# Kernel tuning notes

Hardware: AMD Instinct MI355X
Metric: run time of the kernel (lower is better)

Reference implementation:

```python
import jax, jax.numpy as jnp
import numpy as np

N, E, H, HEADS, NC, BLK = 100000, 1600000, 128, 4, 8192, 128

def _layernorm(x, g, b, eps=1e-5):
    m = jnp.mean(x, axis=-1, keepdims=True)
    v = jnp.var(x, axis=-1, keepdims=True)
    return (x - m) * jax.lax.rsqrt(v + eps) * g + b

def setup_inputs() -> dict:
    key = jax.random.key(0)
    ks = jax.random.split(key, 24)
    s = 0.05
    p = lambda k, shp: jax.random.normal(k, shp, jnp.float32) * s
    return {
        'x': jax.random.normal(ks[0], (N, H), jnp.float32),
        'ea': jax.random.normal(ks[1], (E, H), jnp.float32),
        # GINEConv edge linear (edge_dim -> hidden)
        'We': p(ks[2], (H, H)), 'be_': p(ks[3], (H,)),
        # GINEConv mlp: Linear(H,H) -> ReLU -> Linear(H,H)
        'W1': p(ks[4], (H, H)), 'b1': p(ks[5], (H,)),
        'W2': p(ks[6], (H, H)), 'b2': p(ks[7], (H,)),
        'ln1_g': jnp.ones((H,), jnp.float32), 'ln1_b': jnp.zeros((H,), jnp.float32),
        # MultiheadAttention packed qkv + out proj
        'in_w': p(ks[8], (3 * H, H)), 'in_b': p(ks[9], (3 * H,)),
        'out_w': p(ks[10], (H, H)), 'out_b': p(ks[11], (H,)),
        'ln2_g': jnp.ones((H,), jnp.float32), 'ln2_b': jnp.zeros((H,), jnp.float32),
        # FFN: Linear(H,2H) -> ReLU -> Linear(2H,H)
        'f1_w': p(ks[12], (2 * H, H)), 'f1_b': p(ks[13], (2 * H,)),
        'f2_w': p(ks[14], (H, 2 * H)), 'f2_b': p(ks[15], (H,)),
        'ei': jax.random.randint(ks[16], (2, E), 0, N, jnp.int64),
        'chem_idx': jnp.arange(NC, dtype=jnp.int64),
        'B': BLK,
    }

def reference(x, ea, We, be_, W1, b1, W2, b2, ln1_g, ln1_b, in_w, in_b,
              out_w, out_b, ln2_g, ln2_b, f1_w, f1_b, f2_w, f2_b,
              ei, chem_idx, B):
    n = x.shape[0]
    # ---- GINEConv: out_i = mlp((1+eps)*x_i + sum_j relu(x_j + lin(e_ji))), eps=0 ----
    src, dst = ei[0], ei[1]
    msg = jax.nn.relu(x[src] + ea @ We.T + be_)          # [E, H]
    agg = jax.ops.segment_sum(msg, dst, num_segments=n)  # [N, H]
    h = agg + x
    h = jax.nn.relu(h @ W1.T + b1) @ W2.T + b2
    x = _layernorm(x + h, ln1_g, ln1_b)
    # ---- chunked self-attention over chem nodes (chunks of size B) ----
    xc = x[chem_idx].reshape(-1, B, x.shape[-1])         # [nc, B, H]
    nc, _, hid = xc.shape
    dh = hid // HEADS
    qkv = xc @ in_w.T + in_b                             # [nc, B, 3H]
    q, k, v = jnp.split(qkv, 3, axis=-1)
    sp = lambda t: t.reshape(nc, B, HEADS, dh)
    att = jax.nn.softmax(jnp.einsum('bqhd,bkhd->bhqk', sp(q), sp(k)) * (1.0 / np.sqrt(dh)).astype(np.float32), axis=-1)
    o = jnp.einsum('bhqk,bkhd->bqhd', att, sp(v)).reshape(nc, B, hid)
    xc = xc + (o @ out_w.T + out_b)                      # residual inside BlockMHA
    xc = xc.reshape(-1, hid)
    # ---- FFN on chem subset ----
    h2 = _layernorm(xc, ln2_g, ln2_b)
    xc = xc + (jax.nn.relu(h2 @ f1_w.T + f1_b) @ f2_w.T + f2_b)
    return x.at[chem_idx].set(xc)
```

## Files before the change

### kernel.cpp

```cpp
#include <hip/hip_runtime.h>
#include <hip/hip_bf16.h>
#include <math.h>

typedef __attribute__((ext_vector_type(8))) __bf16 bf16x8;
typedef __attribute__((ext_vector_type(4))) float f32x4;
typedef __attribute__((ext_vector_type(4))) unsigned short u16x4;

#define HD  128
#define LDP 136

__device__ __forceinline__ unsigned short f2bf(float f) {
  __bf16 h = (__bf16)f;
  union { __bf16 h; unsigned short u; } v; v.h = h; return v.u;
}
__device__ __forceinline__ float bf2f(unsigned short h) {
  union { unsigned u; float f; } v; v.u = ((unsigned)h) << 16; return v.f;
}

__device__ __forceinline__ int idx_at(const void* p, long long i, int is64) {
  if (is64) return (int)((const long long*)p)[i];
  return ((const int*)p)[i];
}

__device__ __forceinline__ void mfma_tile_128(const unsigned short* a_s,
                                              const unsigned short* w_s,
                                              int w, int l15, int lg,
                                              f32x4 acc[2][8]) {
#pragma unroll
  for (int kk = 0; kk < 4; ++kk) {
    bf16x8 a[2], b[8];
#pragma unroll
    for (int mt = 0; mt < 2; ++mt)
      a[mt] = *(const bf16x8*)&a_s[(w * 32 + mt * 16 + l15) * LDP + kk * 32 + lg * 8];
#pragma unroll
    for (int nt = 0; nt < 8; ++nt)
      b[nt] = *(const bf16x8*)&w_s[(nt * 16 + l15) * LDP + kk * 32 + lg * 8];
#pragma unroll
    for (int mt = 0; mt < 2; ++mt)
#pragma unroll
      for (int nt = 0; nt < 8; ++nt)
        acc[mt][nt] = __builtin_amdgcn_mfma_f32_16x16x32_bf16(a[mt], b[nt], acc[mt][nt], 0, 0, 0);
  }
}

__device__ __forceinline__ void stage_f32(unsigned short* dst, const float* src,
                                          long long src_ld, int tid) {
  for (int i = tid; i < 128 * 32; i += 256) {
    int r = i >> 5, c = (i & 31) << 2;
    float4 f = *(const float4*)&src[(long long)r * src_ld + c];
    u16x4 h = { f2bf(f.x), f2bf(f.y), f2bf(f.z), f2bf(f.w) };
    *(u16x4*)&dst[r * LDP + c] = h;
  }
}

__global__ void detect_idx_kernel(const void* __restrict__ ei, int E, int N,
                                  int* __restrict__ flag) {
  if (threadIdx.x == 0 && blockIdx.x == 0) {
    const long long* p = (const long long*)ei;
    int is64 = 1;
    long long step = E / 64; if (step < 1) step = 1;
    for (int i = 0; i < 64; ++i) {
      long long v = p[i * step];
      if (v < 0 || v >= N) { is64 = 0; break; }
    }
    *flag = is64;
  }
}

__global__ __launch_bounds__(256) void hist_kernel(const void* __restrict__ ei,
                                                   const int* __restrict__ flag,
                                                   int* __restrict__ deg, int E) {
  const int is64 = *flag;
  for (long long e = blockIdx.x * 256LL + threadIdx.x; e < E;
       e += (long long)gridDim.x * 256)
    atomicAdd(&deg[idx_at(ei, (long long)E + e, is64)], 1);
}

#define SCH 1024
__global__ __launch_bounds__(256) void scan_a(const int* __restrict__ deg,
                                              int* __restrict__ bsum, int N) {
  const int b = blockIdx.x, t = threadIdx.x;
  int p = 0;
#pragma unroll
  for (int k = 0; k < 4; ++k) {
    int idx = b * SCH + t * 4 + k;
    if (idx < N) p += deg[idx];
  }
  __shared__ int warr[4];
  for (int o = 32; o > 0; o >>= 1) p += __shfl_xor(p, o);
  if ((t & 63) == 0) warr[t >> 6] = p;
  __syncthreads();
  if (t == 0) bsum[b] = warr[0] + warr[1] + warr[2] + warr[3];
}
__global__ void scan_b(int* __restrict__ bsum, int* __restrict__ off, int NB, int N) {
  if (threadIdx.x == 0 && blockIdx.x == 0) {
    int run = 0;
    for (int b = 0; b < NB; ++b) { int t = bsum[b]; bsum[b] = run; run += t; }
    off[N] = run;
  }
}
__global__ __launch_bounds__(256) void scan_c(const int* __restrict__ deg,
                                              const int* __restrict__ bsum,
                                              int* __restrict__ off,
                                              int* __restrict__ cursor, int N) {
  const int b = blockIdx.x, t = threadIdx.x;
  int d[4], s = 0;
#pragma unroll
  for (int k = 0; k < 4; ++k) {
    int idx = b * SCH + t * 4 + k;
    d[k] = (idx < N) ? deg[idx] : 0;
    s += d[k];
  }
  __shared__ int arr[256];
  arr[t] = s;
  __syncthreads();
  for (int stp = 1; stp < 256; stp <<= 1) {
    int v = (t >= stp) ? arr[t - stp] : 0;
    __syncthreads();
    arr[t] += v;
    __syncthreads();
  }
  int base = bsum[b] + arr[t] - s;
  int acc = 0;
#pragma unroll
  for (int k = 0; k < 4; ++k) {
    int idx = b * SCH + t * 4 + k;
    if (idx < N) { off[idx] = base + acc; cursor[idx] = base + acc; }
    acc += d[k];
  }
}

__global__ __launch_bounds__(256, 3) void edge_kernel4(
    const float* __restrict__ x, const float* __restrict__ ea,
    const float* __restrict__ We, const float* __restrict__ be,
    const void* __restrict__ ei, const int* __restrict__ flag,
    int* __restrict__ cursor, unsigned short* __restrict__ msg, int E, int N) {
  __shared__ unsigned short we_s[128 * LDP];
  __shared__ int s_src[128];
  __shared__ int s_pos[128];
  const int tid = threadIdx.x;
  const long long e0 = (long long)blockIdx.x * 128;
  const int is64 = *flag;

  if (tid < 128) {
    long long e = e0 + tid;
    int s = 0, p = 0;
    if (e < E) {
      s = idx_at(ei, e, is64);
      int d = idx_at(ei, (long long)E + e, is64);
      p = atomicAdd(&cursor[d], 1);
    }
    s_src[tid] = s; s_pos[tid] = p;
  }

  const int lane = tid & 63, w = tid >> 6;
  const int l15 = lane & 15, lg = lane >> 4;

  float4 af[2][4][2];
#pragma unroll
  for (int mt = 0; mt < 2; ++mt) {
    long long row = e0 + w * 32 + mt * 16 + l15;
    const float* src = &ea[(row < E ? row : e0) * HD + lg * 8];
#pragma unroll
    for (int kk = 0; kk < 4; ++kk) {
      af[mt][kk][0] = *(const float4*)&src[kk * 32];
      af[mt][kk][1] = *(const float4*)&src[kk * 32 + 4];
    }
  }

  for (int i = tid; i < 128 * 32; i += 256) {
    int r = i >> 5, c = (i & 31) << 2;
    float4 g = *(const float4*)&We[r * HD + c];
    u16x4 hw = { f2bf(g.x), f2bf(g.y), f2bf(g.z), f2bf(g.w) };
    *(u16x4*)&we_s[r * LDP + c] = hw;
  }

  bf16x8 a[2][4];
#pragma unroll
  for (int mt = 0; mt < 2; ++mt)
#pragma unroll
    for (int kk = 0; kk < 4; ++kk) {
      float4 f0 = af[mt][kk][0], f1 = af[mt][kk][1];
      bf16x8 t;
      t[0] = (__bf16)f0.x; t[1] = (__bf16)f0.y; t[2] = (__bf16)f0.z; t[3] = (__bf16)f0.w;
      t[4] = (__bf16)f1.x; t[5] = (__bf16)f1.y; t[6] = (__bf16)f1.z; t[7] = (__bf16)f1.w;
      a[mt][kk] = t;
    }
  __syncthreads();

  f32x4 acc[2][8];
#pragma unroll
  for (int mt = 0; mt < 2; ++mt)
#pragma unroll
    for (int nt = 0; nt < 8; ++nt) acc[mt][nt] = (f32x4){0.f, 0.f, 0.f, 0.f};

#pragma unroll
  for (int kk = 0; kk < 4; ++kk) {
    bf16x8 b[8];
#pragma unroll
    for (int nt = 0; nt < 8; ++nt)
      b[nt] = *(const bf16x8*)&we_s[(nt * 16 + l15) * LDP + kk * 32 + lg * 8];
#pragma unroll
    for (int mt = 0; mt < 2; ++mt)
#pragma unroll
      for (int nt = 0; nt < 8; ++nt)
        acc[mt][nt] = __builtin_amdgcn_mfma_f32_16x16x32_bf16(a[mt][kk], b[nt], acc[mt][nt], 0, 0, 0);
  }

  float bev[8];
#pragma unroll
  for (int nt = 0; nt < 8; ++nt) bev[nt] = be[nt * 16 + l15];
  __syncthreads();

#pragma unroll
  for (int mt = 0; mt < 2; ++mt) {
#pragma unroll
    for (int r = 0; r < 4; ++r) {
      int m = w * 32 + mt * 16 + lg * 4 + r;
      if (e0 + m >= E) continue;
      const float* xrow = x + (size_t)s_src[m] * HD;
#pragma unroll
      for (int nt = 0; nt < 8; ++nt) {
        int n = nt * 16 + l15;
        float val = acc[mt][nt][r] + bev[nt] + xrow[n];
        we_s[m * LDP + n] = f2bf(val > 0.f ? val : 0.f);
      }
    }
  }
  __syncthreads();
  for (int i = tid; i < 128 * 16; i += 256) {
    int r = i >> 4, sg = i & 15;
    if (e0 + r >= E) continue;
    *(float4*)&msg[(size_t)s_pos[r] * 128 + sg * 8] = *(const float4*)&we_s[r * LDP + sg * 8];
  }
}

__global__ __launch_bounds__(256) void node_kernel2(
    const float* __restrict__ x, float* __restrict__ xo,
    const int* __restrict__ off, const unsigned short* __restrict__ msg,
    const float* __restrict__ W1, const float* __restrict__ b1,
    const float* __restrict__ W2, const float* __restrict__ b2,
    const float* __restrict__ g1, const float* __restrict__ bt1, int N) {
  __shared__ char smem[2 * 128 * LDP * 2];
  unsigned short* a_s = (unsigned short*)smem;
  unsigned short* w_s = (unsigned short*)smem + 128 * LDP;
  float* y_s = (float*)smem;
  const int tid = threadIdx.x;
  const long long r0 = (long long)blockIdx.x * 128;

  const int grp = tid >> 4, li = tid & 15;
  for (int r = grp; r < 128; r += 16) {
    long long gr = r0 + r;
    float a8[8] = {0.f, 0.f, 0.f, 0.f, 0.f, 0.f, 0.f, 0.f};
    if (gr < N) {
      float4 x0 = *(const float4*)&x[(size_t)gr * HD + li * 8];
      float4 x1 = *(const float4*)&x[(size_t)gr * HD + li * 8 + 4];
      a8[0] = x0.x; a8[1] = x0.y; a8[2] = x0.z; a8[3] = x0.w;
      a8[4] = x1.x; a8[5] = x1.y; a8[6] = x1.z; a8[7] = x1.w;
      const int j0 = off[gr], j1 = off[gr + 1];
      int j = j0;
      for (; j + 1 < j1; j += 2) {
        const u16x4* p0 = (const u16x4*)&msg[(size_t)j * 128 + li * 8];
        const u16x4* p1 = (const u16x4*)&msg[(size_t)(j + 1) * 128 + li * 8];
        u16x4 v0 = p0[0], v1 = p0[1], v2 = p1[0], v3 = p1[1];
#pragma unroll
        for (int k = 0; k < 4; ++k) {
          a8[k]     += bf2f(v0[k]) + bf2f(v2[k]);
          a8[4 + k] += bf2f(v1[k]) + bf2f(v3[k]);
        }
      }
      if (j < j1) {
        const u16x4* p0 = (const u16x4*)&msg[(size_t)j * 128 + li * 8];
        u16x4 v0 = p0[0], v1 = p0[1];
#pragma unroll
        for (int k = 0; k < 4; ++k) { a8[k] += bf2f(v0[k]); a8[4 + k] += bf2f(v1[k]); }
      }
    }
    u16x4 h0 = { f2bf(a8[0]), f2bf(a8[1]), f2bf(a8[2]), f2bf(a8[3]) };
    u16x4 h1 = { f2bf(a8[4]), f2bf(a8[5]), f2bf(a8[6]), f2bf(a8[7]) };
    *(u16x4*)&a_s[r * LDP + li * 8] = h0;
    *(u16x4*)&a_s[r * LDP + li * 8 + 4] = h1;
  }
  stage_f32(w_s, W1, HD, tid);
  __syncthreads();

  const int lane = tid & 63, w = tid >> 6;
  const int l15 = lane & 15, lg = lane >> 4;
  f32x4 acc[2][8];
#pragma unroll
  for (int mt = 0; mt < 2; ++mt)
#pragma unroll
    for (int nt = 0; nt < 8; ++nt) acc[mt][nt] = (f32x4){0.f, 0.f, 0.f, 0.f};
  mfma_tile_128(a_s, w_s, w, l15, lg, acc);
  __syncthreads();

#pragma unroll
  for (int mt = 0; mt < 2; ++mt)
#pragma unroll
    for (int r = 0; r < 4; ++r) {
      int m = w * 32 + mt * 16 + lg * 4 + r;
#pragma unroll
      for (int nt = 0; nt < 8; ++nt) {
        int n = nt * 16 + l15;
        float t = acc[mt][nt][r] + b1[n];
        a_s[m * LDP + n] = f2bf(t > 0.f ? t : 0.f);
      }
    }
  stage_f32(w_s, W2, HD, tid);
  __syncthreads();

  f32x4 acc2[2][8];
#pragma unroll
  for (int mt = 0; mt < 2; ++mt)
#pragma unroll
    for (int nt = 0; nt < 8; ++nt) acc2[mt][nt] = (f32x4){0.f, 0.f, 0.f, 0.f};
  mfma_tile_128(a_s, w_s, w, l15, lg, acc2);
  __syncthreads();

#pragma unroll
  for (int mt = 0; mt < 2; ++mt)
#pragma unroll
    for (int r = 0; r < 4; ++r) {
      int m = w * 32 + mt * 16 + lg * 4 + r;
      if (r0 + m < N) {
#pragma unroll
        for (int nt = 0; nt < 8; ++nt) {
          int n = nt * 16 + l15;
          y_s[m * 132 + n] = x[(r0 + m) * HD + n] + acc2[mt][nt][r] + b2[n];
        }
      }
    }
  __syncthreads();

  for (int row = w; row < 128; row += 4) {
    if (r0 + row >= N) continue;
    float v1 = y_s[row * 132 + lane], v2 = y_s[row * 132 + 64 + lane];
    float s = v1 + v2, sq = v1 * v1 + v2 * v2;
    for (int o = 32; o > 0; o >>= 1) { s += __shfl_xor(s, o); sq += __shfl_xor(sq, o); }
    float mean = s * (1.f / 128.f);
    float var = sq * (1.f / 128.f) - mean * mean;
    float rs = rsqrtf(var + 1e-5f);
    xo[(r0 + row) * HD + lane]      = (v1 - mean) * rs * g1[lane] + bt1[lane];
    xo[(r0 + row) * HD + 64 + lane] = (v2 - mean) * rs * g1[lane + 64] + bt1[lane + 64];
  }
}

__global__ __launch_bounds__(256) void edge_kernel(
    const float* __restrict__ x, const float* __restrict__ ea,
    const float* __restrict__ We, const float* __restrict__ be,
    const void* __restrict__ ei, const int* __restrict__ flag,
    float* __restrict__ agg, int E, int N) {
  __shared__ unsigned short ea_s[128 * LDP];
  __shared__ unsigned short we_s[128 * LDP];
  __shared__ int s_src[128];
  __shared__ int s_dst[128];
  const int tid = threadIdx.x;
  const long long e0 = (long long)blockIdx.x * 128;
  const int is64 = *flag;
  if (tid < 128) {
    long long e = e0 + tid;
    int s = 0, d = 0;
    if (e < E) { s = idx_at(ei, e, is64); d = idx_at(ei, (long long)E + e, is64); }
    s_src[tid] = s; s_dst[tid] = d;
  }
  for (int i = tid; i < 128 * 32; i += 256) {
    int r = i >> 5, c = (i & 31) << 2;
    float4 f = {0.f, 0.f, 0.f, 0.f};
    if (e0 + r < E) f = *(const float4*)&ea[(e0 + r) * HD + c];
    u16x4 h = { f2bf(f.x), f2bf(f.y), f2bf(f.z), f2bf(f.w) };
    *(u16x4*)&ea_s[r * LDP + c] = h;
    float4 g = *(const float4*)&We[r * HD + c];
    u16x4 hw = { f2bf(g.x), f2bf(g.y), f2bf(g.z), f2bf(g.w) };
    *(u16x4*)&we_s[r * LDP + c] = hw;
  }
  __syncthreads();
  const int lane = tid & 63, w = tid >> 6;
  const int l15 = lane & 15, lg = lane >> 4;
  f32x4 acc[2][8];
#pragma unroll
  for (int mt = 0; mt < 2; ++mt)
#pragma unroll
    for (int nt = 0; nt < 8; ++nt) acc[mt][nt] = (f32x4){0.f, 0.f, 0.f, 0.f};
  mfma_tile_128(ea_s, we_s, w, l15, lg, acc);
  float bev[8];
#pragma unroll
  for (int nt = 0; nt < 8; ++nt) bev[nt] = be[nt * 16 + l15];
#pragma unroll
  for (int mt = 0; mt < 2; ++mt) {
#pragma unroll
    for (int r = 0; r < 4; ++r) {
      int m = w * 32 + mt * 16 + lg * 4 + r;
      if (e0 + m >= E) continue;
      const float* xrow = x + (size_t)s_src[m] * HD;
      float* arow = agg + (size_t)s_dst[m] * HD;
#pragma unroll
      for (int nt = 0; nt < 8; ++nt) {
        int n = nt * 16 + l15;
        float val = acc[mt][nt][r] + bev[nt] + xrow[n];
        if (val > 0.f) unsafeAtomicAdd(&arow[n], val);
      }
    }
  }
}

__global__ __launch_bounds__(256) void node_kernel(
    const float* __restrict__ x, float* xo,
    const float* __restrict__ W1, const float* __restrict__ b1,
    const float* __restrict__ W2, const float* __restrict__ b2,
    const float* __restrict__ g1, const float* __restrict__ bt1, int N) {
  __shared__ char smem[2 * 128 * LDP * 2];
  unsigned short* a_s = (unsigned short*)smem;
  unsigned short* w_s = (unsigned short*)smem + 128 * LDP;
  float* y_s = (float*)smem;
  const int tid = threadIdx.x;
  const long long r0 = (long long)blockIdx.x * 128;
  for (int i = tid; i < 128 * 32; i += 256) {
    int r = i >> 5, c = (i & 31) << 2;
    float4 f = {0.f, 0.f, 0.f, 0.f};
    if (r0 + r < N) {
      float4 xa = *(const float4*)&x[(r0 + r) * HD + c];
      float4 ag = *(const float4*)&xo[(r0 + r) * HD + c];
      f.x = xa.x + ag.x; f.y = xa.y + ag.y; f.z = xa.z + ag.z; f.w = xa.w + ag.w;
    }
    u16x4 h = { f2bf(f.x), f2bf(f.y), f2bf(f.z), f2bf(f.w) };
    *(u16x4*)&a_s[r * LDP + c] = h;
    float4 g = *(const float4*)&W1[r * HD + c];
    u16x4 hw = { f2bf(g.x), f2bf(g.y), f2bf(g.z), f2bf(g.w) };
    *(u16x4*)&w_s[r * LDP + c] = hw;
  }
  __syncthreads();
  const int lane = tid & 63, w = tid >> 6;
  const int l15 = lane & 15, lg = lane >> 4;
  f32x4 acc[2][8];
#pragma unroll
  for (int mt = 0; mt < 2; ++mt)
#pragma unroll
    for (int nt = 0; nt < 8; ++nt) acc[mt][nt] = (f32x4){0.f, 0.f, 0.f, 0.f};
  mfma_tile_128(a_s, w_s, w, l15, lg, acc);
  __syncthreads();
#pragma unroll
  for (int mt = 0; mt < 2; ++mt)
#pragma unroll
    for (int r = 0; r < 4; ++r) {
      int m = w * 32 + mt * 16 + lg * 4 + r;
#pragma unroll
      for (int nt = 0; nt < 8; ++nt) {
        int n = nt * 16 + l15;
        float t = acc[mt][nt][r] + b1[n];
        a_s[m * LDP + n] = f2bf(t > 0.f ? t : 0.f);
      }
    }
  stage_f32(w_s, W2, HD, tid);
  __syncthreads();
  f32x4 acc2[2][8];
#pragma unroll
  for (int mt = 0; mt < 2; ++mt)
#pragma unroll
    for (int nt = 0; nt < 8; ++nt) acc2[mt][nt] = (f32x4){0.f, 0.f, 0.f, 0.f};
  mfma_tile_128(a_s, w_s, w, l15, lg, acc2);
  __syncthreads();
#pragma unroll
  for (int mt = 0; mt < 2; ++mt)
#pragma unroll
    for (int r = 0; r < 4; ++r) {
      int m = w * 32 + mt * 16 + lg * 4 + r;
      if (r0 + m < N) {
#pragma unroll
        for (int nt = 0; nt < 8; ++nt) {
          int n = nt * 16 + l15;
          y_s[m * 132 + n] = x[(r0 + m) * HD + n] + acc2[mt][nt][r] + b2[n];
        }
      }
    }
  __syncthreads();
  for (int row = w; row < 128; row += 4) {
    if (r0 + row >= N) continue;
    float v1 = y_s[row * 132 + lane], v2 = y_s[row * 132 + 64 + lane];
    float s = v1 + v2, sq = v1 * v1 + v2 * v2;
    for (int o = 32; o > 0; o >>= 1) { s += __shfl_xor(s, o); sq += __shfl_xor(sq, o); }
    float mean = s * (1.f / 128.f);
    float var = sq * (1.f / 128.f) - mean * mean;
    float rs = rsqrtf(var + 1e-5f);
    xo[(r0 + row) * HD + lane]      = (v1 - mean) * rs * g1[lane] + bt1[lane];
    xo[(r0 + row) * HD + 64 + lane] = (v2 - mean) * rs * g1[lane + 64] + bt1[lane + 64];
  }
}

__global__ __launch_bounds__(256) void qkv_kernel(
    const float* __restrict__ xo, const float* __restrict__ in_w,
    const float* __restrict__ in_b, const void* __restrict__ chem,
    const int* __restrict__ flag, float* __restrict__ qkv) {
  __shared__ unsigned short a_s[128 * LDP];
  __shared__ unsigned short w_s[128 * LDP];
  __shared__ int s_row[128];
  const int tid = threadIdx.x;
  const int chunk = blockIdx.x, sec = blockIdx.y;
  const int is64 = *flag;
  if (tid < 128) s_row[tid] = idx_at(chem, (long long)chunk * 128 + tid, is64);
  __syncthreads();
  for (int i = tid; i < 128 * 32; i += 256) {
    int r = i >> 5, c = (i & 31) << 2;
    float4 f = *(const float4*)&xo[(size_t)s_row[r] * HD + c];
    u16x4 h = { f2bf(f.x), f2bf(f.y), f2bf(f.z), f2bf(f.w) };
    *(u16x4*)&a_s[r * LDP + c] = h;
    float4 g = *(const float4*)&in_w[(size_t)(sec * 128 + r) * HD + c];
    u16x4 hw = { f2bf(g.x), f2bf(g.y), f2bf(g.z), f2bf(g.w) };
    *(u16x4*)&w_s[r * LDP + c] = hw;
  }
  __syncthreads();
  const int lane = tid & 63, w = tid >> 6;
  const int l15 = lane & 15, lg = lane >> 4;
  f32x4 acc[2][8];
#pragma unroll
  for (int mt = 0; mt < 2; ++mt)
#pragma unroll
    for (int nt = 0; nt < 8; ++nt) acc[mt][nt] = (f32x4){0.f, 0.f, 0.f, 0.f};
  mfma_tile_128(a_s, w_s, w, l15, lg, acc);
#pragma unroll
  for (int mt = 0; mt < 2; ++mt)
#pragma unroll
    for (int r = 0; r < 4; ++r) {
      int m = w * 32 + mt * 16 + lg * 4 + r;
#pragma unroll
      for (int nt = 0; nt < 8; ++nt) {
        int n = nt * 16 + l15;
        qkv[(size_t)(chunk * 128 + m) * 384 + sec * 128 + n] = acc[mt][nt][r] + in_b[sec * 128 + n];
      }
    }
}

__global__ __launch_bounds__(128) void attn_kernel(const float* __restrict__ qkv,
                                                   float* __restrict__ o) {
  __shared__ float k_s[128 * 32];
  __shared__ float v_s[128 * 32];
  const int tid = threadIdx.x;
  const int chunk = blockIdx.x, h = blockIdx.y;
  const float scale = 0.1767766952966369f;
  for (int i = tid; i < 128 * 32; i += 128) {
    int r = i >> 5, d = i & 31;
    k_s[i] = qkv[(size_t)(chunk * 128 + r) * 384 + 128 + h * 32 + d];
    v_s[i] = qkv[(size_t)(chunk * 128 + r) * 384 + 256 + h * 32 + d];
  }
  float qr[32];
  const int m = tid;
#pragma unroll
  for (int d = 0; d < 32; ++d)
    qr[d] = qkv[(size_t)(chunk * 128 + m) * 384 + h * 32 + d] * scale;
  __syncthreads();
  float mx = -1e30f, sm = 0.f;
  for (int j = 0; j < 128; ++j) {
    float s = 0.f;
#pragma unroll
    for (int d = 0; d < 32; ++d) s += qr[d] * k_s[j * 32 + d];
    if (s > mx) { sm = sm * __expf(mx - s); mx = s; }
    sm += __expf(s - mx);
  }
  const float inv = 1.f / sm;
  float ov[32];
#pragma unroll
  for (int d = 0; d < 32; ++d) ov[d] = 0.f;
  for (int j = 0; j < 128; ++j) {
    float s = 0.f;
#pragma unroll
    for (int d = 0; d < 32; ++d) s += qr[d] * k_s[j * 32 + d];
    float p = __expf(s - mx) * inv;
#pragma unroll
    for (int d = 0; d < 32; ++d) ov[d] += p * v_s[j * 32 + d];
  }
#pragma unroll
  for (int d = 0; d < 32; ++d)
    o[(size_t)(chunk * 128 + m) * HD + h * 32 + d] = ov[d];
}

__global__ __launch_bounds__(256) void oproj_kernel(
    const float* __restrict__ xo, const float* __restrict__ o,
    const float* __restrict__ Wo, const float* __restrict__ bo,
    const float* __restrict__ g2, const float* __restrict__ bt2,
    const void* __restrict__ chem, const int* __restrict__ flag,
    float* __restrict__ xc2, unsigned short* __restrict__ h2b) {
  __shared__ char smem[2 * 128 * LDP * 2];
  unsigned short* a_s = (unsigned short*)smem;
  unsigned short* w_s = (unsigned short*)smem + 128 * LDP;
  float* y_s = (float*)smem;
  __shared__ int s_row[128];
  const int tid = threadIdx.x;
  const int chunk = blockIdx.x;
  const int is64 = *flag;
  if (tid < 128) s_row[tid] = idx_at(chem, (long long)chunk * 128 + tid, is64);
  stage_f32(a_s, o + (size_t)chunk * 128 * HD, HD, tid);
  stage_f32(w_s, Wo, HD, tid);
  __syncthreads();
  const int lane = tid & 63, w = tid >> 6;
  const int l15 = lane & 15, lg = lane >> 4;
  f32x4 acc[2][8];
#pragma unroll
  for (int mt = 0; mt < 2; ++mt)
#pragma unroll
    for (int nt = 0; nt < 8; ++nt) acc[mt][nt] = (f32x4){0.f, 0.f, 0.f, 0.f};
  mfma_tile_128(a_s, w_s, w, l15, lg, acc);
  __syncthreads();
#pragma unroll
  for (int mt = 0; mt < 2; ++mt)
#pragma unroll
    for (int r = 0; r < 4; ++r) {
      int m = w * 32 + mt * 16 + lg * 4 + r;
#pragma unroll
      for (int nt = 0; nt < 8; ++nt) {
        int n = nt * 16 + l15;
        y_s[m * 132 + n] = xo[(size_t)s_row[m] * HD + n] + acc[mt][nt][r] + bo[n];
      }
    }
  __syncthreads();
  for (int row = w; row < 128; row += 4) {
    float v1 = y_s[row * 132 + lane], v2 = y_s[row * 132 + 64 + lane];
    float s = v1 + v2, sq = v1 * v1 + v2 * v2;
    for (int o2 = 32; o2 > 0; o2 >>= 1) { s += __shfl_xor(s, o2); sq += __shfl_xor(sq, o2); }
    float mean = s * (1.f / 128.f);
    float var = sq * (1.f / 128.f) - mean * mean;
    float rs = rsqrtf(var + 1e-5f);
    size_t gi = (size_t)(chunk * 128 + row) * HD;
    xc2[gi + lane] = v1; xc2[gi + 64 + lane] = v2;
    h2b[gi + lane]      = f2bf((v1 - mean) * rs * g2[lane] + bt2[lane]);
    h2b[gi + 64 + lane] = f2bf((v2 - mean) * rs * g2[lane + 64] + bt2[lane + 64]);
  }
}

__global__ __launch_bounds__(256) void ffn1_kernel(
    const unsigned short* __restrict__ h2b, const float* __restrict__ f1w,
    const float* __restrict__ f1b, unsigned short* __restrict__ u) {
  __shared__ unsigned short a_s[128 * LDP];
  __shared__ unsigned short w_s[128 * LDP];
  const int tid = threadIdx.x;
  const int chunk = blockIdx.x, sec = blockIdx.y;
  for (int i = tid; i < 128 * 32; i += 256) {
    int r = i >> 5, c = (i & 31) << 2;
    *(u16x4*)&a_s[r * LDP + c] = *(const u16x4*)&h2b[(size_t)(chunk * 128 + r) * HD + c];
  }
  stage_f32(w_s, f1w + (size_t)sec * 128 * HD, HD, tid);
  __syncthreads();
  const int lane = tid & 63, w = tid >> 6;
  const int l15 = lane & 15, lg = lane >> 4;
  f32x4 acc[2][8];
#pragma unroll
  for (int mt = 0; mt < 2; ++mt)
#pragma unroll
    for (int nt = 0; nt < 8; ++nt) acc[mt][nt] = (f32x4){0.f, 0.f, 0.f, 0.f};
  mfma_tile_128(a_s, w_s, w, l15, lg, acc);
#pragma unroll
  for (int mt = 0; mt < 2; ++mt)
#pragma unroll
    for (int r = 0; r < 4; ++r) {
      int m = w * 32 + mt * 16 + lg * 4 + r;
#pragma unroll
      for (int nt = 0; nt < 8; ++nt) {
        int n = nt * 16 + l15;
        float t = acc[mt][nt][r] + f1b[sec * 128 + n];
        u[(size_t)(chunk * 128 + m) * 256 + sec * 128 + n] = f2bf(t > 0.f ? t : 0.f);
      }
    }
}

__global__ __launch_bounds__(256) void ffn2_kernel(
    const unsigned short* __restrict__ u, const float* __restrict__ f2w,
    const float* __restrict__ f2b, const float* __restrict__ xc2,
    const void* __restrict__ chem, const int* __restrict__ flag,
    float* __restrict__ out) {
  __shared__ unsigned short a_s[128 * LDP];
  __shared__ unsigned short w_s[128 * LDP];
  __shared__ int s_row[128];
  const int tid = threadIdx.x;
  const int chunk = blockIdx.x;
  const int is64 = *flag;
  if (tid < 128) s_row[tid] = idx_at(chem, (long long)chunk * 128 + tid, is64);
  const int lane = tid & 63, w = tid >> 6;
  const int l15 = lane & 15, lg = lane >> 4;
  f32x4 acc[2][8];
#pragma unroll
  for (int mt = 0; mt < 2; ++mt)
#pragma unroll
    for (int nt = 0; nt < 8; ++nt) acc[mt][nt] = (f32x4){0.f, 0.f, 0.f, 0.f};
  for (int half = 0; half < 2; ++half) {
    __syncthreads();
    for (int i = tid; i < 128 * 32; i += 256) {
      int r = i >> 5, c = (i & 31) << 2;
      *(u16x4*)&a_s[r * LDP + c] =
          *(const u16x4*)&u[(size_t)(chunk * 128 + r) * 256 + half * 128 + c];
      float4 g = *(const float4*)&f2w[(size_t)r * 256 + half * 128 + c];
      u16x4 hw = { f2bf(g.x), f2bf(g.y), f2bf(g.z), f2bf(g.w) };
      *(u16x4*)&w_s[r * LDP + c] = hw;
    }
    __syncthreads();
    mfma_tile_128(a_s, w_s, w, l15, lg, acc);
  }
#pragma unroll
  for (int mt = 0; mt < 2; ++mt)
#pragma unroll
    for (int r = 0; r < 4; ++r) {
      int m = w * 32 + mt * 16 + lg * 4 + r;
#pragma unroll
      for (int nt = 0; nt < 8; ++nt) {
        int n = nt * 16 + l15;
        float val = xc2[(size_t)(chunk * 128 + m) * HD + n] + acc[mt][nt][r] + f2b[n];
        out[(size_t)s_row[m] * HD + n] = val;
      }
    }
}

extern "C" void kernel_launch(void* const* d_in, const int* in_sizes, int n_in,
                              void* d_out, int out_size, void* d_ws, size_t ws_size,
                              hipStream_t stream) {
  const float* x    = (const float*)d_in[0];
  const float* ea   = (const float*)d_in[1];
  const float* We   = (const float*)d_in[2];
  const float* be   = (const float*)d_in[3];
  const float* W1   = (const float*)d_in[4];
  const float* b1   = (const float*)d_in[5];
  const float* W2   = (const float*)d_in[6];
  const float* b2   = (const float*)d_in[7];
  const float* g1   = (const float*)d_in[8];
  const float* bt1  = (const float*)d_in[9];
  const float* in_w = (const float*)d_in[10];
  const float* in_b = (const float*)d_in[11];
  const float* outw = (const float*)d_in[12];
  const float* outb = (const float*)d_in[13];
  const float* g2   = (const float*)d_in[14];
  const float* bt2  = (const float*)d_in[15];
  const float* f1w  = (const float*)d_in[16];
  const float* f1b  = (const float*)d_in[17];
  const float* f2w  = (const float*)d_in[18];
  const float* f2b  = (const float*)d_in[19];
  const void*  ei   = d_in[20];
  const void*  chem = d_in[21];
  const int N  = in_sizes[0] / HD;
  const int E  = in_sizes[1] / HD;
  const int NC = in_sizes[21];
  const int NB = (N + SCH - 1) / SCH;
  float* xo = (float*)d_out;

  char* ws = (char*)d_ws;
  size_t o = 0;
  auto alloc = [&](size_t bytes) { size_t p = o; o = (o + bytes + 255) & ~255ULL; return p; };
  size_t o_qkv  = alloc((size_t)NC * 384 * 4);
  size_t o_obuf = alloc((size_t)NC * 128 * 4);
  size_t o_xc2  = alloc((size_t)NC * 128 * 4);
  size_t o_h2b  = alloc((size_t)NC * 128 * 2);
  size_t o_ubuf = alloc((size_t)NC * 256 * 2);
  size_t o_flag = alloc(4);
  size_t o_deg  = alloc((size_t)N * 4);
  size_t o_off  = alloc((size_t)(N + 1) * 4);
  size_t o_cur  = alloc((size_t)N * 4);
  size_t o_bsum = alloc((size_t)NB * 4);
  size_t o_msg  = alloc((size_t)E * 128 * 2);
  size_t need = o;

  float*          qkv  = (float*)(ws + o_qkv);
  float*          obuf = (float*)(ws + o_obuf);
  float*          xc2  = (float*)(ws + o_xc2);
  unsigned short* h2b  = (unsigned short*)(ws + o_h2b);
  unsigned short* ubuf = (unsigned short*)(ws + o_ubuf);
  int*            flag = (int*)(ws + o_flag);
  int*            deg  = (int*)(ws + o_deg);
  int*            off  = (int*)(ws + o_off);
  int*            cur  = (int*)(ws + o_cur);
  int*            bsum = (int*)(ws + o_bsum);
  unsigned short* msg  = (unsigned short*)(ws + o_msg);

  detect_idx_kernel<<<1, 64, 0, stream>>>(ei, E, N, flag);

  if (ws_size >= need) {
    hipMemsetAsync(deg, 0, (size_t)N * 4, stream);
    hist_kernel<<<dim3(1024), 256, 0, stream>>>(ei, flag, deg, E);
    scan_a<<<dim3(NB), 256, 0, stream>>>(deg, bsum, N);
    scan_b<<<1, 64, 0, stream>>>(bsum, off, NB, N);
    scan_c<<<dim3(NB), 256, 0, stream>>>(deg, bsum, off, cur, N);
    edge_kernel4<<<dim3((E + 127) / 128), 256, 0, stream>>>(x, ea, We, be, ei, flag,
                                                            cur, msg, E, N);
    node_kernel2<<<dim3((N + 127) / 128), 256, 0, stream>>>(x, xo, off, msg, W1, b1,
                                                            W2, b2, g1, bt1, N);
  } else {
    hipMemsetAsync(xo, 0, (size_t)N * HD * sizeof(float), stream);
    edge_kernel<<<dim3((E + 127) / 128), 256, 0, stream>>>(x, ea, We, be, ei, flag, xo, E, N);
    node_kernel<<<dim3((N + 127) / 128), 256, 0, stream>>>(x, xo, W1, b1, W2, b2, g1, bt1, N);
  }

  const int ncs = NC / 128;
  qkv_kernel<<<dim3(ncs, 3), 256, 0, stream>>>(xo, in_w, in_b, chem, flag, qkv);
  attn_kernel<<<dim3(ncs, 4), 128, 0, stream>>>(qkv, obuf);
  oproj_kernel<<<dim3(ncs), 256, 0, stream>>>(xo, obuf, outw, outb, g2, bt2, chem, flag, xc2, h2b);
  ffn1_kernel<<<dim3(ncs, 2), 256, 0, stream>>>(h2b, f1w, f1b, ubuf);
  ffn2_kernel<<<dim3(ncs), 256, 0, stream>>>(ubuf, f2w, f2b, xc2, chem, flag, xo);
}
```

Measured before the change: 807.4 us.

## Pre-convert GINE weights to bf16 once and read node MFMA weights from global

Adds small kernels that convert We, W1 and W2 to bf16 once per call. The edge kernel then copies pre-padded bf16 weights instead of converting fp32 per block. The node kernel reads W1/W2 fragments straight from global memory, drops the weight LDS buffer to raise occupancy, and stores the LayerNorm input in bf16 LDS. It also unrolls the message gather by four. This trades a few extra launches and bf16 rounding of the pre-LayerNorm value (a precision loss) for less per-block conversion work and LDS pressure.

```diff
diff --git a/kernel.cpp b/kernel.cpp
--- a/kernel.cpp
+++ b/kernel.cpp
@@ -43,9 +43,30 @@
   }
 }
 
-__device__ __forceinline__ void stage_f32(unsigned short* dst, const float* src,
-                                          long long src_ld, int tid) {
-  for (int i = tid; i < 128 * 32; i += 256) {
+__device__ __forceinline__ void mfma_tile_gb(const unsigned short* a_s,
+                                             const unsigned short* Wb,
+                                             int w, int l15, int lg,
+                                             f32x4 acc[2][8]) {
+#pragma unroll
+  for (int kk = 0; kk < 4; ++kk) {
+    bf16x8 a[2], b[8];
+#pragma unroll
+    for (int mt = 0; mt < 2; ++mt)
+      a[mt] = *(const bf16x8*)&a_s[(w * 32 + mt * 16 + l15) * LDP + kk * 32 + lg * 8];
+#pragma unroll
+    for (int nt = 0; nt < 8; ++nt)
+      b[nt] = *(const bf16x8*)&Wb[(nt * 16 + l15) * 128 + kk * 32 + lg * 8];
+#pragma unroll
+    for (int mt = 0; mt < 2; ++mt)
+#pragma unroll
+      for (int nt = 0; nt < 8; ++nt)
+        acc[mt][nt] = __builtin_amdgcn_mfma_f32_16x16x32_bf16(a[mt], b[nt], acc[mt][nt], 0, 0, 0);
+  }
+}
+
+__device__ __forceinline__ void stage_f32s(unsigned short* dst, const float* src,
+                                           long long src_ld, int tid, int T) {
+  for (int i = tid; i < 128 * 32; i += T) {
     int r = i >> 5, c = (i & 31) << 2;
     float4 f = *(const float4*)&src[(long long)r * src_ld + c];
     u16x4 h = { f2bf(f.x), f2bf(f.y), f2bf(f.z), f2bf(f.w) };
@@ -67,6 +88,21 @@
   }
 }
 
+__global__ __launch_bounds__(256) void conv_we_kernel(const float* __restrict__ We,
+                                                      unsigned short* __restrict__ we_bf) {
+  int i = blockIdx.x * 256 + threadIdx.x;
+  if (i < 128 * 128) {
+    int r = i >> 7, c = i & 127;
+    we_bf[r * 136 + c] = f2bf(We[i]);
+  }
+}
+__global__ __launch_bounds__(256) void conv_w_kernel(const float* __restrict__ W,
+                                                     unsigned short* __restrict__ out,
+                                                     int n) {
+  int i = blockIdx.x * 256 + threadIdx.x;
+  if (i < n) out[i] = f2bf(W[i]);
+}
+
 __global__ __launch_bounds__(256) void hist_kernel(const void* __restrict__ ei,
                                                    const int* __restrict__ flag,
                                                    int* __restrict__ deg, int E) {
@@ -130,11 +166,11 @@
   }
 }
 
-__global__ __launch_bounds__(256, 3) void edge_kernel4(
+__global__ __launch_bounds__(256, 4) void edge_kernel6(
     const float* __restrict__ x, const float* __restrict__ ea,
-    const float* __restrict__ We, const float* __restrict__ be,
+    const unsigned short* __restrict__ we_bf, const float* __restrict__ be,
     const void* __restrict__ ei, const int* __restrict__ flag,
-    int* __restrict__ cursor, unsigned short* __restrict__ msg, int E, int N) {
+    int* __restrict__ cursor, unsigned short* __restrict__ msg, int E) {
   __shared__ unsigned short we_s[128 * LDP];
   __shared__ int s_src[128];
   __shared__ int s_pos[128];
@@ -168,11 +204,9 @@
     }
   }
 
-  for (int i = tid; i < 128 * 32; i += 256) {
-    int r = i >> 5, c = (i & 31) << 2;
-    float4 g = *(const float4*)&We[r * HD + c];
-    u16x4 hw = { f2bf(g.x), f2bf(g.y), f2bf(g.z), f2bf(g.w) };
-    *(u16x4*)&we_s[r * LDP + c] = hw;
+  for (int i = tid; i < 2048; i += 256) {
+    int r = i >> 4, c = (i & 15) << 3;
+    *(float4*)&we_s[r * LDP + c] = *(const float4*)&we_bf[r * 136 + c];
   }
 
   bf16x8 a[2][4];
@@ -235,16 +269,13 @@
   }
 }
 
-__global__ __launch_bounds__(256) void node_kernel2(
+__global__ __launch_bounds__(256, 3) void node_kernel7(
     const float* __restrict__ x, float* __restrict__ xo,
     const int* __restrict__ off, const unsigned short* __restrict__ msg,
-    const float* __restrict__ W1, const float* __restrict__ b1,
-    const float* __restrict__ W2, const float* __restrict__ b2,
+    const unsigned short* __restrict__ W1b, const float* __restrict__ b1,
+    const unsigned short* __restrict__ W2b, const float* __restrict__ b2,
     const float* __restrict__ g1, const float* __restrict__ bt1, int N) {
-  __shared__ char smem[2 * 128 * LDP * 2];
-  unsigned short* a_s = (unsigned short*)smem;
-  unsigned short* w_s = (unsigned short*)smem + 128 * LDP;
-  float* y_s = (float*)smem;
+  __shared__ unsigned short a_s[128 * LDP];
   const int tid = threadIdx.x;
   const long long r0 = (long long)blockIdx.x * 128;
 
@@ -259,17 +290,20 @@
       a8[4] = x1.x; a8[5] = x1.y; a8[6] = x1.z; a8[7] = x1.w;
       const int j0 = off[gr], j1 = off[gr + 1];
       int j = j0;
-      for (; j + 1 < j1; j += 2) {
+      for (; j + 3 < j1; j += 4) {
         const u16x4* p0 = (const u16x4*)&msg[(size_t)j * 128 + li * 8];
         const u16x4* p1 = (const u16x4*)&msg[(size_t)(j + 1) * 128 + li * 8];
+        const u16x4* p2 = (const u16x4*)&msg[(size_t)(j + 2) * 128 + li * 8];
+        const u16x4* p3 = (const u16x4*)&msg[(size_t)(j + 3) * 128 + li * 8];
         u16x4 v0 = p0[0], v1 = p0[1], v2 = p1[0], v3 = p1[1];
+        u16x4 v4 = p2[0], v5 = p2[1], v6 = p3[0], v7 = p3[1];
 #pragma unroll
         for (int k = 0; k < 4; ++k) {
-          a8[k]     += bf2f(v0[k]) + bf2f(v2[k]);
-          a8[4 + k] += bf2f(v1[k]) + bf2f(v3[k]);
+          a8[k]     += (bf2f(v0[k]) + bf2f(v2[k])) + (bf2f(v4[k]) + bf2f(v6[k]));
+          a8[4 + k] += (bf2f(v1[k]) + bf2f(v3[k])) + (bf2f(v5[k]) + bf2f(v7[k]));
         }
       }
-      if (j < j1) {
+      for (; j < j1; ++j) {
         const u16x4* p0 = (const u16x4*)&msg[(size_t)j * 128 + li * 8];
         u16x4 v0 = p0[0], v1 = p0[1];
 #pragma unroll
@@ -281,7 +315,6 @@
     *(u16x4*)&a_s[r * LDP + li * 8] = h0;
     *(u16x4*)&a_s[r * LDP + li * 8 + 4] = h1;
   }
-  stage_f32(w_s, W1, HD, tid);
   __syncthreads();
 
   const int lane = tid & 63, w = tid >> 6;
@@ -291,7 +324,7 @@
   for (int mt = 0; mt < 2; ++mt)
 #pragma unroll
     for (int nt = 0; nt < 8; ++nt) acc[mt][nt] = (f32x4){0.f, 0.f, 0.f, 0.f};
-  mfma_tile_128(a_s, w_s, w, l15, lg, acc);
+  mfma_tile_gb(a_s, W1b, w, l15, lg, acc);
   __syncthreads();
 
 #pragma unroll
@@ -306,7 +339,6 @@
         a_s[m * LDP + n] = f2bf(t > 0.f ? t : 0.f);
       }
     }
-  stage_f32(w_s, W2, HD, tid);
   __syncthreads();
 
   f32x4 acc2[2][8];
@@ -314,7 +346,7 @@
   for (int mt = 0; mt < 2; ++mt)
 #pragma unroll
     for (int nt = 0; nt < 8; ++nt) acc2[mt][nt] = (f32x4){0.f, 0.f, 0.f, 0.f};
-  mfma_tile_128(a_s, w_s, w, l15, lg, acc2);
+  mfma_tile_gb(a_s, W2b, w, l15, lg, acc2);
   __syncthreads();
 
 #pragma unroll
@@ -326,7 +358,7 @@
 #pragma unroll
         for (int nt = 0; nt < 8; ++nt) {
           int n = nt * 16 + l15;
-          y_s[m * 132 + n] = x[(r0 + m) * HD + n] + acc2[mt][nt][r] + b2[n];
+          a_s[m * LDP + n] = f2bf(x[(r0 + m) * HD + n] + acc2[mt][nt][r] + b2[n]);
         }
       }
     }
@@ -334,7 +366,7 @@
 
   for (int row = w; row < 128; row += 4) {
     if (r0 + row >= N) continue;
-    float v1 = y_s[row * 132 + lane], v2 = y_s[row * 132 + 64 + lane];
+    float v1 = bf2f(a_s[row * LDP + lane]), v2 = bf2f(a_s[row * LDP + 64 + lane]);
     float s = v1 + v2, sq = v1 * v1 + v2 * v2;
     for (int o = 32; o > 0; o >>= 1) { s += __shfl_xor(s, o); sq += __shfl_xor(sq, o); }
     float mean = s * (1.f / 128.f);
@@ -450,7 +482,7 @@
         a_s[m * LDP + n] = f2bf(t > 0.f ? t : 0.f);
       }
     }
-  stage_f32(w_s, W2, HD, tid);
+  stage_f32s(w_s, W2, HD, tid, 256);
   __syncthreads();
   f32x4 acc2[2][8];
 #pragma unroll
@@ -587,8 +619,8 @@
   const int chunk = blockIdx.x;
   const int is64 = *flag;
   if (tid < 128) s_row[tid] = idx_at(chem, (long long)chunk * 128 + tid, is64);
-  stage_f32(a_s, o + (size_t)chunk * 128 * HD, HD, tid);
-  stage_f32(w_s, Wo, HD, tid);
+  stage_f32s(a_s, o + (size_t)chunk * 128 * HD, HD, tid, 256);
+  stage_f32s(w_s, Wo, HD, tid, 256);
   __syncthreads();
   const int lane = tid & 63, w = tid >> 6;
   const int l15 = lane & 15, lg = lane >> 4;
@@ -636,7 +668,7 @@
     int r = i >> 5, c = (i & 31) << 2;
     *(u16x4*)&a_s[r * LDP + c] = *(const u16x4*)&h2b[(size_t)(chunk * 128 + r) * HD + c];
   }
-  stage_f32(w_s, f1w + (size_t)sec * 128 * HD, HD, tid);
+  stage_f32s(w_s, f1w + (size_t)sec * 128 * HD, HD, tid, 256);
   __syncthreads();
   const int lane = tid & 63, w = tid >> 6;
   const int l15 = lane & 15, lg = lane >> 4;
@@ -746,6 +778,9 @@
   size_t o_h2b  = alloc((size_t)NC * 128 * 2);
   size_t o_ubuf = alloc((size_t)NC * 256 * 2);
   size_t o_flag = alloc(4);
+  size_t o_webf = alloc(128 * 136 * 2);
+  size_t o_w1b  = alloc(128 * 128 * 2);
+  size_t o_w2b  = alloc(128 * 128 * 2);
   size_t o_deg  = alloc((size_t)N * 4);
   size_t o_off  = alloc((size_t)(N + 1) * 4);
   size_t o_cur  = alloc((size_t)N * 4);
@@ -759,6 +794,9 @@
   unsigned short* h2b  = (unsigned short*)(ws + o_h2b);
   unsigned short* ubuf = (unsigned short*)(ws + o_ubuf);
   int*            flag = (int*)(ws + o_flag);
+  unsigned short* webf = (unsigned short*)(ws + o_webf);
+  unsigned short* w1b  = (unsigned short*)(ws + o_w1b);
+  unsigned short* w2b  = (unsigned short*)(ws + o_w2b);
   int*            deg  = (int*)(ws + o_deg);
   int*            off  = (int*)(ws + o_off);
   int*            cur  = (int*)(ws + o_cur);
@@ -773,10 +811,13 @@
     scan_a<<<dim3(NB), 256, 0, stream>>>(deg, bsum, N);
     scan_b<<<1, 64, 0, stream>>>(bsum, off, NB, N);
     scan_c<<<dim3(NB), 256, 0, stream>>>(deg, bsum, off, cur, N);
-    edge_kernel4<<<dim3((E + 127) / 128), 256, 0, stream>>>(x, ea, We, be, ei, flag,
-                                                            cur, msg, E, N);
-    node_kernel2<<<dim3((N + 127) / 128), 256, 0, stream>>>(x, xo, off, msg, W1, b1,
-                                                            W2, b2, g1, bt1, N);
+    conv_we_kernel<<<dim3(64), 256, 0, stream>>>(We, webf);
+    conv_w_kernel<<<dim3(64), 256, 0, stream>>>(W1, w1b, 128 * 128);
+    conv_w_kernel<<<dim3(64), 256, 0, stream>>>(W2, w2b, 128 * 128);
+    edge_kernel6<<<dim3((E + 127) / 128), 256, 0, stream>>>(x, ea, webf, be, ei, flag,
+                                                            cur, msg, E);
+    node_kernel7<<<dim3((N + 127) / 128), 256, 0, stream>>>(x, xo, off, msg, w1b, b1,
+                                                            w2b, b2, g1, bt1, N);
   } else {
     hipMemsetAsync(xo, 0, (size_t)N * HD * sizeof(float), stream);
     edge_kernel<<<dim3((E + 127) / 128), 256, 0, stream>>>(x, ea, We, be, ei, flag, xo, E, N);
```

After: 789.9 us. 1.02x faster.
